# Optimization experiments

Hardware: AMD Instinct MI355X
Metric: run time of the kernel (lower is better)

The kernel has to match this reference:

```python
import jax, jax.numpy as jnp
import numpy as np

H = 8  # num_heads
NEG = -1000000.0

def _ln(x, g, b):
    m = jnp.mean(x, axis=-1, keepdims=True)
    v = jnp.var(x, axis=-1, keepdims=True)
    return (x - m) / jnp.sqrt(v + 1e-5) * g + b


def setup_inputs() -> dict:
    key = jax.random.key(0)
    ks = jax.random.split(key, 24)
    B, T, D = 8, 1024, 1024
    Lt, Nt, K, Rt, E = 768, 77, 2, 512, 2048
    s = 0.02
    r = lambda i, shape: s * jax.random.normal(ks[i], shape, jnp.float32)
    return {
        "x": jax.random.normal(ks[0], (B, T, D), jnp.float32),
        "xf": jax.random.normal(ks[1], (B, Nt, Lt), jnp.float32),
        "emb": jax.random.normal(ks[2], (B, E), jnp.float32),
        "src_mask": jnp.ones((B, T, 1), jnp.float32),
        "cond_type": jax.random.randint(ks[3], (B, 1, 1), 0, 100),
        "re_motion": jax.random.normal(ks[4], (B, K, Rt, D), jnp.float32),
        "re_text": jax.random.normal(ks[5], (B, K, 1, D), jnp.float32),
        "re_mask": jnp.ones((B, K, Rt), jnp.float32),
        "ln_g": jnp.ones((D,)), "ln_b": jnp.zeros((D,)),
        "tln_g": jnp.ones((Lt,)), "tln_b": jnp.zeros((Lt,)),
        "rn1_g": jnp.ones((2 * D,)), "rn1_b": jnp.zeros((2 * D,)),
        "rn2_g": jnp.ones((D,)), "rn2_b": jnp.zeros((D,)),
        "Wq": r(6, (D, D)), "bq": jnp.zeros((D,)),
        "Wkt": r(7, (Lt, D)), "bkt": jnp.zeros((D,)),
        "Wvt": r(8, (Lt, D)), "bvt": jnp.zeros((D,)),
        "Wkm": r(9, (D, D)), "bkm": jnp.zeros((D,)),
        "Wvm": r(10, (D, D)), "bvm": jnp.zeros((D,)),
        "Wkr": r(11, (2 * D, D)), "bkr": jnp.zeros((D,)),
        "Wvr": r(12, (D, D)), "bvr": jnp.zeros((D,)),  # zero-init in original; random here for nontrivial math
        "We": r(13, (E, 2 * D)), "be": jnp.zeros((2 * D,)),
        "sln_g": jnp.ones((D,)), "sln_b": jnp.zeros((D,)),
        "Wo": r(14, (D, D)), "bo": jnp.zeros((D,)),  # zero-init in original
    }


def reference(x, xf, emb, src_mask, cond_type, re_motion, re_text, re_mask,
              ln_g, ln_b, tln_g, tln_b, rn1_g, rn1_b, rn2_g, rn2_b,
              Wq, bq, Wkt, bkt, Wvt, bvt, Wkm, bkm, Wvm, bvm,
              Wkr, bkr, Wvr, bvr, We, be, sln_g, sln_b, Wo, bo):
    B, T, D = x.shape
    K, Rt = re_motion.shape[1], re_motion.shape[2]

    norm_x = _ln(x, ln_g, ln_b)
    norm_xf = _ln(xf, tln_g, tln_b)
    query = norm_x @ Wq + bq  # (B,T,D)

    text_ct = (cond_type % 10 > 0).astype(x.dtype)   # (B,1,1)
    retr_ct = (cond_type // 10 > 0).astype(x.dtype)  # (B,1,1)
    re_mask_r = re_mask.reshape(B, -1, 1)            # (B,K*Rt,1)

    # retrieval key features: concat(motion, repeated text) along channels
    re_text_rep = jnp.broadcast_to(re_text, (B, K, Rt, D))
    re_feat_key = jnp.concatenate([re_motion, re_text_rep], axis=-1).reshape(B, -1, 2 * D)

    key_text = norm_xf @ Wkt + bkt + (1.0 - text_ct) * NEG
    key_retr = _ln(re_feat_key, rn1_g, rn1_b) @ Wkr + bkr \
        + (1.0 - retr_ct) * NEG + (1.0 - re_mask_r) * NEG
    key_motion = norm_x @ Wkm + bkm + (1.0 - src_mask) * NEG
    key = jnp.concatenate([key_text, key_retr, key_motion], axis=1)  # (B,N,D)
    N = key.shape[1]

    q = jax.nn.softmax(query.reshape(B, T, H, -1), axis=-1)  # softmax over head dim
    k = jax.nn.softmax(key.reshape(B, N, H, -1), axis=1)     # softmax over tokens

    value_text = (norm_xf @ Wvt + bvt) * text_ct
    value_retr = (_ln(re_motion.reshape(B, -1, D), rn2_g, rn2_b) @ Wvr + bvr) * retr_ct * re_mask_r
    value_motion = (norm_x @ Wvm + bvm) * src_mask
    v = jnp.concatenate([value_text, value_retr, value_motion], axis=1).reshape(B, N, H, -1)

    att = jnp.einsum('bnhd,bnhl->bhdl', k, v)          # (B,H,dh,dh)
    y = jnp.einsum('bthd,bhdl->bthl', q, att).reshape(B, T, D)

    # StylizationBlock: FiLM from time embedding, then zero-init out proj (eval: dropout = id)
    eo = jax.nn.silu(emb) @ We + be                    # (B,2D)
    scale, shift = jnp.split(eo[:, None, :], 2, axis=2)
    h = _ln(y, sln_g, sln_b) * (1.0 + scale) + shift
    h = jax.nn.silu(h) @ Wo + bo
    return x + h
```

## Files before the change

### kernel.cpp

```cpp
#include <hip/hip_runtime.h>
#include <hip/hip_bf16.h>
#include <math.h>

using bf16 = __hip_bfloat16;

typedef short s16x8 __attribute__((ext_vector_type(8)));
typedef short s16x4 __attribute__((ext_vector_type(4)));
typedef float f32x4 __attribute__((ext_vector_type(4)));

constexpr int Bc = 8, Tc = 1024, Dc = 1024, Hc = 8;
constexpr int NTc = 77, LTc = 768, KRc = 1024, Nc = 2125, Ec = 2048;
constexpr float NEGC = -1000000.0f;

constexpr int NP = 2128;
constexpr long SKT = (long)Dc * NP;

constexpr long F_STATS1 = 0;
constexpr long F_STATS2 = F_STATS1 + 16384;
constexpr long F_KEYADD = F_STATS2 + 16384;
constexpr long F_VALMUL = F_KEYADD + 17000;
constexpr long F_SILU   = F_VALMUL + 17000;
constexpr long F_EO     = F_SILU + 16384;
constexpr long F_ATT    = F_EO + 16384;
constexpr long F_END    = F_ATT + 1048576;
constexpr long KT_SZ   = (long)Bc * Dc * NP;
constexpr long B_NORMX = 0;
constexpr long B_Q     = B_NORMX + 8388608;
constexpr long B_KT    = B_Q + 8388608;
constexpr long B_VT    = B_KT + KT_SZ;
constexpr long B_NXF   = B_VT + KT_SZ;
constexpr long B_WQ    = B_NXF + 473088;
constexpr long B_WKM   = B_WQ + 1048576;
constexpr long B_WVM   = B_WKM + 1048576;
constexpr long B_WKT   = B_WVM + 1048576;
constexpr long B_WVT   = B_WKT + 786432;
constexpr long B_WKR   = B_WVT + 786432;
constexpr long B_WVR   = B_WKR + 2097152;
constexpr long B_WO    = B_WVR + 1048576;
constexpr long B_END   = B_WO + 1048576;
constexpr size_t WS_NEED = (size_t)F_END * 4 + (size_t)B_END * 2;

__device__ __forceinline__ float b2f(bf16 v) { return __bfloat162float(v); }
__device__ __forceinline__ bf16 f2b(float v) { return __float2bfloat16(v); }
__device__ __forceinline__ short f2s(float v) {
    bf16 h = __float2bfloat16(v);
    return *reinterpret_cast<short*>(&h);
}
__device__ __forceinline__ float us2f(unsigned short u) {
    bf16 h = *reinterpret_cast<bf16*>(&u);
    return __bfloat162float(h);
}
__device__ __forceinline__ void storef(float* p, float v) { *p = v; }
__device__ __forceinline__ void storef(bf16* p, float v) { *p = __float2bfloat16(v); }

typedef __attribute__((address_space(1))) const unsigned int gu32;
typedef __attribute__((address_space(3))) unsigned int lu32;
__device__ __forceinline__ void gl_lds16(const void* g, void* l) {
    __builtin_amdgcn_global_load_lds((gu32*)g, (lu32*)l, 16, 0, 0);
}

__device__ __forceinline__ float2 block_sum2(float s, float s2) {
    #pragma unroll
    for (int off = 32; off > 0; off >>= 1) {
        s  += __shfl_down(s, off, 64);
        s2 += __shfl_down(s2, off, 64);
    }
    __shared__ float sh[4], sh2[4];
    int w = threadIdx.x >> 6, lane = threadIdx.x & 63;
    if (lane == 0) { sh[w] = s; sh2[w] = s2; }
    __syncthreads();
    s = sh[0] + sh[1] + sh[2] + sh[3];
    s2 = sh2[0] + sh2[1] + sh2[2] + sh2[3];
    return make_float2(s, s2);
}

template <typename TO>
__global__ __launch_bounds__(256) void ln_rows(const float* __restrict__ in,
                                               const float* __restrict__ g,
                                               const float* __restrict__ b,
                                               TO* __restrict__ out, int C) {
    long row = blockIdx.x;
    const float* x = in + row * (long)C;
    TO* o = out + row * (long)C;
    float s = 0.f, s2 = 0.f;
    for (int c = threadIdx.x; c < C; c += 256) { float v = x[c]; s += v; s2 += v * v; }
    float2 r = block_sum2(s, s2);
    float mean = r.x / C;
    float var = r.y / C - mean * mean;
    float inv = rsqrtf(var + 1e-5f);
    for (int c = threadIdx.x; c < C; c += 256)
        storef(&o[c], (x[c] - mean) * inv * g[c] + b[c]);
}

__global__ __launch_bounds__(256) void ln_stats_both(const float* __restrict__ motion,
                                                     const float* __restrict__ text,
                                                     float* __restrict__ stats1,
                                                     float* __restrict__ stats2) {
    long row = blockIdx.x;
    const float* m = motion + row * 1024;
    const float* tx = text + (row >> 9) * 1024;
    float s = 0.f, s2 = 0.f;
    for (int c = threadIdx.x; c < 1024; c += 256) { float v = m[c]; s += v; s2 += v * v; }
    float2 rm = block_sum2(s, s2);
    __syncthreads();
    float st = 0.f, st2 = 0.f;
    for (int c = threadIdx.x; c < 1024; c += 256) { float v = tx[c]; st += v; st2 += v * v; }
    float2 rt = block_sum2(st, st2);
    if (threadIdx.x == 0) {
        float mean2 = rm.x / 1024.f;
        float var2 = rm.y / 1024.f - mean2 * mean2;
        stats2[2 * row] = mean2;
        stats2[2 * row + 1] = rsqrtf(var2 + 1e-5f);
        float mean1 = (rm.x + rt.x) / 2048.f;
        float var1 = (rm.y + rt.y) / 2048.f - mean1 * mean1;
        stats1[2 * row] = mean1;
        stats1[2 * row + 1] = rsqrtf(var1 + 1e-5f);
    }
}

__device__ __forceinline__ s16x4 pack4(float4 v, float mean, float rstd, float4 g, float4 b) {
    s16x4 o;
    o[0] = f2s((v.x - mean) * rstd * g.x + b.x);
    o[1] = f2s((v.y - mean) * rstd * g.y + b.y);
    o[2] = f2s((v.z - mean) * rstd * g.z + b.z);
    o[3] = f2s((v.w - mean) * rstd * g.w + b.w);
    return o;
}
__global__ __launch_bounds__(256) void materialize_ren(
    const float* __restrict__ motion, const float* __restrict__ text,
    const float* __restrict__ stats1, const float* __restrict__ stats2,
    const float* __restrict__ g1, const float* __restrict__ b1,
    const float* __restrict__ g2, const float* __restrict__ b2,
    bf16* __restrict__ ren1, bf16* __restrict__ ren2) {
    long row = blockIdx.x;
    int c = threadIdx.x * 4;
    const float* mrow = motion + row * 1024;
    const float* trow = text + (row >> 9) * 1024;
    float m1 = stats1[2 * row], r1 = stats1[2 * row + 1];
    float m2 = stats2[2 * row], r2 = stats2[2 * row + 1];
    float4 mv = *(const float4*)(mrow + c);
    float4 tv = *(const float4*)(trow + c);
    float4 g1m = *(const float4*)(g1 + c),        b1m = *(const float4*)(b1 + c);
    float4 g1t = *(const float4*)(g1 + 1024 + c), b1t = *(const float4*)(b1 + 1024 + c);
    float4 g2m = *(const float4*)(g2 + c),        b2m = *(const float4*)(b2 + c);
    *(s16x4*)((short*)ren1 + row * 2048 + c)        = pack4(mv, m1, r1, g1m, b1m);
    *(s16x4*)((short*)ren1 + row * 2048 + 1024 + c) = pack4(tv, m1, r1, g1t, b1t);
    *(s16x4*)((short*)ren2 + row * 1024 + c)        = pack4(mv, m2, r2, g2m, b2m);
}

__global__ __launch_bounds__(256) void prep_masks(const int* __restrict__ cond_type,
                                                  const float* __restrict__ src_mask,
                                                  const float* __restrict__ re_mask,
                                                  float* __restrict__ key_add,
                                                  float* __restrict__ val_mul) {
    int idx = blockIdx.x * 256 + threadIdx.x;
    if (idx >= Bc * Nc) return;
    int b = idx / Nc, n = idx % Nc;
    int ct = cond_type[b];
    float text_ct = ((ct % 10) > 0) ? 1.f : 0.f;
    float retr_ct = ((ct / 10) > 0) ? 1.f : 0.f;
    float add, mul;
    if (n < NTc) {
        add = (1.f - text_ct) * NEGC; mul = text_ct;
    } else if (n < NTc + KRc) {
        float rm = re_mask[b * KRc + (n - NTc)];
        add = (1.f - retr_ct) * NEGC + (1.f - rm) * NEGC;
        mul = retr_ct * rm;
    } else {
        float sm = src_mask[b * Tc + (n - NTc - KRc)];
        add = (1.f - sm) * NEGC; mul = sm;
    }
    key_add[idx] = add;
    val_mul[idx] = mul;
}

__global__ __launch_bounds__(256) void zero_tail(bf16* __restrict__ vT) {
    int row = blockIdx.x * 256 + threadIdx.x;
    if (row >= Bc * Dc) return;
    bf16* p = vT + (long)row * NP + Nc;
    p[0] = f2b(0.f); p[1] = f2b(0.f); p[2] = f2b(0.f);
}

__global__ __launch_bounds__(256) void transpose_all(
    const float* __restrict__ Wq,  const float* __restrict__ Wkt,
    const float* __restrict__ Wvt, const float* __restrict__ Wkm,
    const float* __restrict__ Wvm, const float* __restrict__ Wkr,
    const float* __restrict__ Wvr, const float* __restrict__ Wo,
    short* __restrict__ WtQ,  short* __restrict__ WtKT,
    short* __restrict__ WtVT, short* __restrict__ WtKM,
    short* __restrict__ WtVM, short* __restrict__ WtKR,
    short* __restrict__ WtVR, short* __restrict__ WtO) {
    __shared__ float t[32][33];
    int sy = blockIdx.y;
    const float* W; short* Wt; int K; int ky;
    if (sy < 32)       { W = Wq;  Wt = WtQ;  K = 1024; ky = sy; }
    else if (sy < 56)  { W = Wkt; Wt = WtKT; K = 768;  ky = sy - 32; }
    else if (sy < 80)  { W = Wvt; Wt = WtVT; K = 768;  ky = sy - 56; }
    else if (sy < 112) { W = Wkm; Wt = WtKM; K = 1024; ky = sy - 80; }
    else if (sy < 144) { W = Wvm; Wt = WtVM; K = 1024; ky = sy - 112; }
    else if (sy < 208) { W = Wkr; Wt = WtKR; K = 2048; ky = sy - 144; }
    else if (sy < 240) { W = Wvr; Wt = WtVR; K = 1024; ky = sy - 208; }
    else               { W = Wo;  Wt = WtO;  K = 1024; ky = sy - 240; }
    int n0 = blockIdx.x * 32, k0 = ky * 32;
    int tx = threadIdx.x & 31, ty = threadIdx.x >> 5;
    #pragma unroll
    for (int i = 0; i < 4; ++i)
        t[ty + i * 8][tx] = W[(long)(k0 + ty + i * 8) * 1024 + n0 + tx];
    __syncthreads();
    #pragma unroll
    for (int i = 0; i < 4; ++i)
        Wt[(long)(n0 + ty + i * 8) * K + k0 + tx] = f2s(t[tx][ty + i * 8]);
}

constexpr int LDK = 64;

__global__ __launch_bounds__(256) void gemm_mega(
    const short* __restrict__ norm_x, const short* __restrict__ ren1,
    const short* __restrict__ nxf,
    const short* __restrict__ WtQKVM, const short* __restrict__ WtKR,
    const short* __restrict__ WtTXT,
    const float* __restrict__ bq, const float* __restrict__ bkm,
    const float* __restrict__ bvm, const float* __restrict__ bkr,
    const float* __restrict__ bkt, const float* __restrict__ bvt,
    const float* __restrict__ key_add, const float* __restrict__ val_mul,
    bf16* __restrict__ q16, bf16* __restrict__ kT, bf16* __restrict__ vT) {
    int jid = blockIdx.x;
    int sect, tm, tn, K, M, lda, bb = 0;
    const short* A; const short* Bt;
    if (jid < 512) {
        sect = 0;
        int s = (jid & 7) * 64 + (jid >> 3);
        bb = s >> 6; int r = s & 63;
        tm = (r >> 3) * 128; tn = (r & 7) * 128;
        A = ren1 + (long)bb * KRc * 2048; lda = 2048; K = 2048; M = 1024;
        Bt = WtKR;
    } else if (jid < 2048) {
        sect = 1;
        int l = jid - 512;
        int s = (l & 7) * 192 + (l >> 3);
        tn = (s % 24) * 128; tm = (s / 24) * 128;
        A = norm_x; lda = 1024; K = 1024; M = 8192;
        Bt = WtQKVM;
    } else {
        sect = 2;
        int l = jid - 2048;
        bb = l >> 4; tn = (l & 15) * 128; tm = 0;
        A = nxf + (long)bb * NTc * LTc; lda = 768; K = 768; M = 77;
        Bt = WtTXT;
    }
    const int ldb = lda;
    const bool swap_ops = !(sect == 1 && tn < 1024);

    __shared__ __align__(16) short As[128 * LDK];
    __shared__ __align__(16) short Bs[128 * LDK];

    int tid = threadIdx.x;
    int lane = tid & 63, wid = tid >> 6;
    int wi = wid >> 1, wj = wid & 1;
    int l16 = lane & 15, quad = lane >> 4;

    f32x4 acc[4][4];
    #pragma unroll
    for (int i = 0; i < 4; ++i)
        #pragma unroll
        for (int j = 0; j < 4; ++j)
            acc[i][j] = (f32x4){0.f, 0.f, 0.f, 0.f};

    auto issue = [&](int k0) {
        #pragma unroll
        for (int p = 0; p < 4; ++p) {
            int e = p * 256 + tid;
            int row = e >> 3, c8 = e & 7;
            int gm = tm + row;
            if (gm >= M) gm = M - 1;
            gl_lds16(A + (long)gm * lda + k0 + c8 * 8, &As[row * LDK + c8 * 8]);
            gl_lds16(Bt + (long)(tn + row) * ldb + k0 + c8 * 8, &Bs[row * LDK + c8 * 8]);
        }
    };

    issue(0);
    int kt = 0;
    while (true) {
        __syncthreads();
        #pragma unroll
        for (int kk = 0; kk < 2; ++kk) {
            s16x8 af[4], bfr[4];
            #pragma unroll
            for (int i = 0; i < 4; ++i)
                af[i] = *(const s16x8*)&As[(wi * 64 + i * 16 + l16) * LDK + kk * 32 + quad * 8];
            #pragma unroll
            for (int j = 0; j < 4; ++j)
                bfr[j] = *(const s16x8*)&Bs[(wj * 64 + j * 16 + l16) * LDK + kk * 32 + quad * 8];
            if (swap_ops) {
                #pragma unroll
                for (int i = 0; i < 4; ++i)
                    #pragma unroll
                    for (int j = 0; j < 4; ++j)
                        acc[i][j] = __builtin_amdgcn_mfma_f32_16x16x32_bf16(bfr[j], af[i], acc[i][j], 0, 0, 0);
            } else {
                #pragma unroll
                for (int i = 0; i < 4; ++i)
                    #pragma unroll
                    for (int j = 0; j < 4; ++j)
                        acc[i][j] = __builtin_amdgcn_mfma_f32_16x16x32_bf16(af[i], bfr[j], acc[i][j], 0, 0, 0);
            }
        }
        int nxt = kt + 64;
        if (nxt >= K) break;
        __syncthreads();
        issue(nxt);
        kt = nxt;
    }

    if (sect == 1 && tn < 1024) {
        #pragma unroll
        for (int i = 0; i < 4; ++i) {
            #pragma unroll
            for (int r = 0; r < 4; ++r) {
                int gm = tm + wi * 64 + i * 16 + quad * 4 + r;
                #pragma unroll
                for (int j = 0; j < 4; ++j) {
                    int gn = tn + wj * 64 + j * 16 + l16;
                    q16[(long)gm * Dc + gn] = f2b(acc[i][j][r] + bq[gn]);
                }
            }
        }
    } else if (sect == 1) {
        int sec = tn >> 10, fn0 = tn & 1023;
        const float* bias = (sec == 1) ? bkm : bvm;
        bf16* C = (sec == 1) ? kT : vT;
        #pragma unroll
        for (int j = 0; j < 4; ++j) {
            #pragma unroll
            for (int r = 0; r < 4; ++r) {
                int feat = fn0 + wj * 64 + j * 16 + quad * 4 + r;
                float bf_ = bias[feat];
                #pragma unroll
                for (int i = 0; i < 4; ++i) {
                    int gm = tm + wi * 64 + i * 16 + l16;
                    int b = gm >> 10, tok = gm & 1023;
                    int mi = b * Nc + NTc + KRc + tok;
                    float v = acc[i][j][r] + bf_;
                    if (sec == 1) v += key_add[mi];
                    else          v *= val_mul[mi];
                    C[(long)b * SKT + (long)feat * NP + NTc + KRc + tok] = f2b(v);
                }
            }
        }
    } else if (sect == 0) {
        const float* rmask = key_add + bb * Nc + NTc;
        bf16* C = kT + (long)bb * SKT + NTc;
        #pragma unroll
        for (int j = 0; j < 4; ++j) {
            #pragma unroll
            for (int r = 0; r < 4; ++r) {
                int feat = tn + wj * 64 + j * 16 + quad * 4 + r;
                float bf_ = bkr[feat];
                #pragma unroll
                for (int i = 0; i < 4; ++i) {
                    int tok = tm + wi * 64 + i * 16 + l16;
                    C[(long)feat * NP + tok] = f2b(acc[i][j][r] + bf_ + rmask[tok]);
                }
            }
        }
    } else {
        int sec = tn >> 10, fn0 = tn & 1023;
        const float* bias = sec ? bvt : bkt;
        const float* rmask = (sec ? val_mul : key_add) + bb * Nc;
        bf16* C = (sec ? vT : kT) + (long)bb * SKT;
        #pragma unroll
        for (int j = 0; j < 4; ++j) {
            #pragma unroll
            for (int r = 0; r < 4; ++r) {
                int feat = fn0 + wj * 64 + j * 16 + quad * 4 + r;
                float bf_ = bias[feat];
                #pragma unroll
                for (int i = 0; i < 4; ++i) {
                    int tok = wi * 64 + i * 16 + l16;
                    if (tok >= NTc) continue;
                    float v = acc[i][j][r] + bf_;
                    if (sec) v *= rmask[tok];
                    else     v += rmask[tok];
                    C[(long)feat * NP + tok] = f2b(v);
                }
            }
        }
    }
}

__global__ __launch_bounds__(256) void gemm_vr(
    const short* __restrict__ ren2, const short* __restrict__ WtVR,
    const float* __restrict__ bvr, const float* __restrict__ val_mul,
    bf16* __restrict__ vT) {
    int s = (blockIdx.x & 7) * 64 + (blockIdx.x >> 3);
    int b = s >> 6; int r = s & 63;
    const int tm = (r >> 3) * 128;
    const int tn = (r & 7) * 128;
    const short* A = ren2 + (long)b * KRc * 1024;
    const float* rmask = val_mul + b * Nc + NTc;
    bf16* C = vT + (long)b * SKT + NTc;

    __shared__ __align__(16) short As[128 * LDK];
    __shared__ __align__(16) short Bs[128 * LDK];

    int tid = threadIdx.x;
    int lane = tid & 63, wid = tid >> 6;
    int wi = wid >> 1, wj = wid & 1;
    int l16 = lane & 15, quad = lane >> 4;

    f32x4 acc[4][4];
    #pragma unroll
    for (int i = 0; i < 4; ++i)
        #pragma unroll
        for (int j = 0; j < 4; ++j)
            acc[i][j] = (f32x4){0.f, 0.f, 0.f, 0.f};

    auto issue = [&](int k0) {
        #pragma unroll
        for (int p = 0; p < 4; ++p) {
            int e = p * 256 + tid;
            int row = e >> 3, c8 = e & 7;
            gl_lds16(A + (long)(tm + row) * 1024 + k0 + c8 * 8, &As[row * LDK + c8 * 8]);
            gl_lds16(WtVR + (long)(tn + row) * 1024 + k0 + c8 * 8, &Bs[row * LDK + c8 * 8]);
        }
    };

    issue(0);
    int kt = 0;
    while (true) {
        __syncthreads();
        #pragma unroll
        for (int kk = 0; kk < 2; ++kk) {
            s16x8 af[4], bfr[4];
            #pragma unroll
            for (int i = 0; i < 4; ++i)
                af[i] = *(const s16x8*)&As[(wi * 64 + i * 16 + l16) * LDK + kk * 32 + quad * 8];
            #pragma unroll
            for (int j = 0; j < 4; ++j)
                bfr[j] = *(const s16x8*)&Bs[(wj * 64 + j * 16 + l16) * LDK + kk * 32 + quad * 8];
            #pragma unroll
            for (int i = 0; i < 4; ++i)
                #pragma unroll
                for (int j = 0; j < 4; ++j)
                    acc[i][j] = __builtin_amdgcn_mfma_f32_16x16x32_bf16(bfr[j], af[i], acc[i][j], 0, 0, 0);
        }
        int nxt = kt + 64;
        if (nxt >= 1024) break;
        __syncthreads();
        issue(nxt);
        kt = nxt;
    }

    #pragma unroll
    for (int j = 0; j < 4; ++j) {
        #pragma unroll
        for (int r2 = 0; r2 < 4; ++r2) {
            int feat = tn + wj * 64 + j * 16 + quad * 4 + r2;
            float bf_ = bvr[feat];
            #pragma unroll
            for (int i = 0; i < 4; ++i) {
                int tok = tm + wi * 64 + i * 16 + l16;
                C[(long)feat * NP + tok] = f2b((acc[i][j][r2] + bf_) * rmask[tok]);
            }
        }
    }
}

template <typename TC>
__global__ __launch_bounds__(256) void gemm_bt(
    const short* __restrict__ A, int lda,
    const short* __restrict__ Bt, int ldb,
    const float* __restrict__ bias,
    const float* __restrict__ addC, int ldac,
    TC* __restrict__ C, int ldc, int K) {
    int nx = gridDim.x;
    int nwg = nx * gridDim.y;
    int lin = blockIdx.y * nx + blockIdx.x;
    int bx = blockIdx.x, by = blockIdx.y;
    if ((nwg & 7) == 0) {
        int chunk = nwg >> 3;
        int swz = (lin & 7) * chunk + (lin >> 3);
        bx = swz % nx; by = swz / nx;
    }
    const int tm = by * 128;
    const int tn = bx * 128;

    __shared__ __align__(16) short As[128 * LDK];
    __shared__ __align__(16) short Bs[128 * LDK];

    int tid = threadIdx.x;
    int lane = tid & 63, wid = tid >> 6;
    int wi = wid >> 1, wj = wid & 1;
    int l16 = lane & 15, quad = lane >> 4;

    f32x4 acc[4][4];
    #pragma unroll
    for (int i = 0; i < 4; ++i)
        #pragma unroll
        for (int j = 0; j < 4; ++j)
            acc[i][j] = (f32x4){0.f, 0.f, 0.f, 0.f};

    auto issue = [&](int k0) {
        #pragma unroll
        for (int p = 0; p < 4; ++p) {
            int e = p * 256 + tid;
            int row = e >> 3, c8 = e & 7;
            gl_lds16(A + (long)(tm + row) * lda + k0 + c8 * 8, &As[row * LDK + c8 * 8]);
            gl_lds16(Bt + (long)(tn + row) * ldb + k0 + c8 * 8, &Bs[row * LDK + c8 * 8]);
        }
    };

    issue(0);
    int kt = 0;
    while (true) {
        __syncthreads();
        #pragma unroll
        for (int kk = 0; kk < 2; ++kk) {
            s16x8 af[4], bfr[4];
            #pragma unroll
            for (int i = 0; i < 4; ++i)
                af[i] = *(const s16x8*)&As[(wi * 64 + i * 16 + l16) * LDK + kk * 32 + quad * 8];
            #pragma unroll
            for (int j = 0; j < 4; ++j)
                bfr[j] = *(const s16x8*)&Bs[(wj * 64 + j * 16 + l16) * LDK + kk * 32 + quad * 8];
            #pragma unroll
            for (int i = 0; i < 4; ++i)
                #pragma unroll
                for (int j = 0; j < 4; ++j)
                    acc[i][j] = __builtin_amdgcn_mfma_f32_16x16x32_bf16(af[i], bfr[j], acc[i][j], 0, 0, 0);
        }
        int nxt = kt + 64;
        if (nxt >= K) break;
        __syncthreads();
        issue(nxt);
        kt = nxt;
    }

    #pragma unroll
    for (int i = 0; i < 4; ++i) {
        #pragma unroll
        for (int r = 0; r < 4; ++r) {
            int gm = tm + wi * 64 + i * 16 + quad * 4 + r;
            #pragma unroll
            for (int j = 0; j < 4; ++j) {
                int gn = tn + wj * 64 + j * 16 + l16;
                float v = acc[i][j][r] + bias[gn];
                if (addC) v += addC[(long)gm * ldac + gn];
                storef(&C[(long)gm * ldc + gn], v);
            }
        }
    }
}

__global__ __launch_bounds__(256) void eo_partial(const float* __restrict__ emb,
                                                  const float* __restrict__ We,
                                                  float* __restrict__ part) {
    int nb = blockIdx.x;
    int ks = blockIdx.y;
    int n = nb * 256 + threadIdx.x;
    int k0 = ks * 64;
    __shared__ float a_s[8][64];
    for (int idx = threadIdx.x; idx < 512; idx += 256) {
        int b = idx >> 6, kk = idx & 63;
        float v = emb[b * 2048 + k0 + kk];
        a_s[b][kk] = v / (1.f + expf(-v));
    }
    __syncthreads();
    float acc[8] = {};
    for (int kk = 0; kk < 64; ++kk) {
        float w = We[(long)(k0 + kk) * 2048 + n];
        #pragma unroll
        for (int b = 0; b < 8; ++b) acc[b] = fmaf(a_s[b][kk], w, acc[b]);
    }
    #pragma unroll
    for (int b = 0; b < 8; ++b) part[((long)ks * 8 + b) * 2048 + n] = acc[b];
}

__global__ __launch_bounds__(256) void eo_reduce(const float* __restrict__ part,
                                                 const float* __restrict__ be,
                                                 float* __restrict__ eo) {
    int idx = blockIdx.x * 256 + threadIdx.x;
    int n = idx & 2047, b = idx >> 11;
    float s = be[n];
    #pragma unroll 8
    for (int ks = 0; ks < 32; ++ks) s += part[((long)ks * 8 + b) * 2048 + n];
    eo[idx] = s;
}

__global__ __launch_bounds__(256) void softmax_head(bf16* __restrict__ q) {
    long row = (long)blockIdx.x * 4 + (threadIdx.x >> 6);
    int lane = threadIdx.x & 63;
    bf16* p = q + row * 128 + lane * 2;
    float v0 = b2f(p[0]), v1 = b2f(p[1]);
    float mx = fmaxf(v0, v1);
    #pragma unroll
    for (int off = 32; off > 0; off >>= 1) mx = fmaxf(mx, __shfl_xor(mx, off, 64));
    float e0 = expf(v0 - mx), e1 = expf(v1 - mx);
    float s = e0 + e1;
    #pragma unroll
    for (int off = 32; off > 0; off >>= 1) s += __shfl_xor(s, off, 64);
    float inv = 1.f / s;
    p[0] = f2b(e0 * inv);
    p[1] = f2b(e1 * inv);
}

__global__ __launch_bounds__(256) void ksm_rows(const bf16* __restrict__ kT,
                                                float* __restrict__ cs_m,
                                                float* __restrict__ cs_inv) {
    int row = blockIdx.x * 4 + (threadIdx.x >> 6);
    int lane = threadIdx.x & 63;
    const s16x8* p8 = (const s16x8*)(kT + (long)row * NP);
    float m = -3.0e38f;
    for (int c = lane; c < NP / 8; c += 64) {
        s16x8 raw = p8[c];
        int n0 = c * 8;
        #pragma unroll
        for (int j = 0; j < 8; ++j)
            if (n0 + j < Nc) m = fmaxf(m, us2f((unsigned short)raw[j]));
    }
    #pragma unroll
    for (int off = 32; off > 0; off >>= 1) m = fmaxf(m, __shfl_xor(m, off, 64));
    float s = 0.f;
    for (int c = lane; c < NP / 8; c += 64) {
        s16x8 raw = p8[c];
        int n0 = c * 8;
        #pragma unroll
        for (int j = 0; j < 8; ++j)
            if (n0 + j < Nc) s += __expf(us2f((unsigned short)raw[j]) - m);
    }
    #pragma unroll
    for (int off = 32; off > 0; off >>= 1) s += __shfl_xor(s, off, 64);
    if (lane == 0) { cs_m[row] = m; cs_inv[row] = 1.f / s; }
}

constexpr int ATT_SPLIT = 4;
__global__ __launch_bounds__(256) void att_gemm(const bf16* __restrict__ kTb,
                                                const bf16* __restrict__ vTb,
                                                const float* __restrict__ cs_m,
                                                float* __restrict__ att_part) {
    int bh = blockIdx.x;
    int split = blockIdx.y;
    int b = bh >> 3, h = bh & 7;
    const short* A  = (const short*)kTb + ((long)b * 1024 + h * 128) * NP;
    const short* Bt = (const short*)vTb + ((long)b * 1024 + h * 128) * NP;
    float* ap = att_part + ((long)split * 64 + bh) * 16384;

    __shared__ __align__(16) short As[128 * LDK];
    __shared__ __align__(16) short Bs[128 * LDK];
    __shared__ float ms[128];

    int tid = threadIdx.x;
    if (tid < 128) ms[tid] = cs_m[(long)b * 1024 + h * 128 + tid];

    int lane = tid & 63, wid = tid >> 6;
    int wi = wid >> 1, wj = wid & 1;
    int l16 = lane & 15, quad = lane >> 4;

    f32x4 acc[4][4];
    #pragma unroll
    for (int i = 0; i < 4; ++i)
        #pragma unroll
        for (int j = 0; j < 4; ++j)
            acc[i][j] = (f32x4){0.f, 0.f, 0.f, 0.f};

    uint4 pa[4];
    auto computeA = [&](int k0) {
        #pragma unroll
        for (int p = 0; p < 4; ++p) {
            int e = p * 256 + tid;
            int row = e >> 3, c8 = e & 7;
            int n0 = k0 + c8 * 8;
            union { short s[8]; uint4 u; } pk;
            if (n0 >= Nc) {
                pk.u = (uint4){0u, 0u, 0u, 0u};
            } else {
                float m = ms[row];
                s16x8 raw = *(const s16x8*)(A + (long)row * NP + n0);
                #pragma unroll
                for (int j = 0; j < 8; ++j) {
                    float v = (n0 + j < Nc) ? __expf(us2f((unsigned short)raw[j]) - m) : 0.f;
                    pk.s[j] = f2s(v);
                }
            }
            pa[p] = pk.u;
        }
    };
    auto issueB = [&](int k0) {
        #pragma unroll
        for (int p = 0; p < 4; ++p) {
            int e = p * 256 + tid;
            int row = e >> 3, c8 = e & 7;
            int n0 = k0 + c8 * 8;
            if (n0 > NP - 8) n0 = NP - 8;
            gl_lds16(Bt + (long)row * NP + n0, &Bs[row * LDK + c8 * 8]);
        }
    };
    auto storeA = [&]() {
        #pragma unroll
        for (int p = 0; p < 4; ++p) {
            int e = p * 256 + tid;
            int row = e >> 3, c8 = e & 7;
            *(uint4*)&As[row * LDK + c8 * 8] = pa[p];
        }
    };

    int st = (split < 2) ? split * 9 : 18 + (split - 2) * 8;
    int cnt = (split < 2) ? 9 : 8;
    int kt = st * 64;
    int kend = kt + cnt * 64;

    __syncthreads();
    issueB(kt);
    computeA(kt);
    storeA();
    while (true) {
        __syncthreads();
        #pragma unroll
        for (int kk = 0; kk < 2; ++kk) {
            s16x8 af[4], bfr[4];
            #pragma unroll
            for (int i = 0; i < 4; ++i)
                af[i] = *(const s16x8*)&As[(wi * 64 + i * 16 + l16) * LDK + kk * 32 + quad * 8];
            #pragma unroll
            for (int j = 0; j < 4; ++j)
                bfr[j] = *(const s16x8*)&Bs[(wj * 64 + j * 16 + l16) * LDK + kk * 32 + quad * 8];
            #pragma unroll
            for (int i = 0; i < 4; ++i)
                #pragma unroll
                for (int j = 0; j < 4; ++j)
                    acc[i][j] = __builtin_amdgcn_mfma_f32_16x16x32_bf16(bfr[j], af[i], acc[i][j], 0, 0, 0);
        }
        int nxt = kt + 64;
        if (nxt >= kend) break;
        computeA(nxt);
        __syncthreads();
        issueB(nxt);
        storeA();
        kt = nxt;
    }

    #pragma unroll
    for (int j = 0; j < 4; ++j) {
        #pragma unroll
        for (int r = 0; r < 4; ++r) {
            int l = wj * 64 + j * 16 + quad * 4 + r;
            #pragma unroll
            for (int i = 0; i < 4; ++i) {
                int d = wi * 64 + i * 16 + l16;
                ap[l * 128 + d] = acc[i][j][r];
            }
        }
    }
}

__global__ __launch_bounds__(256) void reduce_att_t(const float* __restrict__ att_part,
                                                    const float* __restrict__ cs_inv,
                                                    bf16* __restrict__ attT) {
    long idx = (long)blockIdx.x * 256 + threadIdx.x;
    if (idx >= (long)64 * 16384) return;
    float s = 0.f;
    #pragma unroll
    for (int sp = 0; sp < ATT_SPLIT; ++sp) s += att_part[(long)sp * 64 * 16384 + idx];
    int bh = (int)(idx >> 14);
    int d = (int)(idx & 127);
    int b = bh >> 3, h = bh & 7;
    attT[idx] = f2b(s * cs_inv[b * Dc + h * 128 + d]);
}

__global__ __launch_bounds__(256) void y_gemm(const bf16* __restrict__ q,
                                              const bf16* __restrict__ attT,
                                              bf16* __restrict__ y) {
    int bh = blockIdx.y;
    int b = bh >> 3, h = bh & 7;
    const short* A  = (const short*)q + (long)b * Tc * Dc + h * 128;
    const short* Bt = (const short*)attT + (long)bh * 16384;
    bf16* yb = y + (long)b * Tc * Dc + h * 128;
    int tm = blockIdx.x * 128;

    __shared__ __align__(16) short As[128 * 128];
    __shared__ __align__(16) short Bs[128 * 128];
    int tid = threadIdx.x;
    #pragma unroll
    for (int p = 0; p < 8; ++p) {
        int e = p * 256 + tid;
        int row = e >> 4, c8 = e & 15;
        gl_lds16(A + (long)(tm + row) * Dc + c8 * 8, &As[row * 128 + c8 * 8]);
        gl_lds16(Bt + row * 128 + c8 * 8, &Bs[row * 128 + c8 * 8]);
    }
    int lane = tid & 63, wid = tid >> 6;
    int wi = wid >> 1, wj = wid & 1;
    int l16 = lane & 15, quad = lane >> 4;
    f32x4 acc[4][4];
    #pragma unroll
    for (int i = 0; i < 4; ++i)
        #pragma unroll
        for (int j = 0; j < 4; ++j)
            acc[i][j] = (f32x4){0.f, 0.f, 0.f, 0.f};
    __syncthreads();
    #pragma unroll
    for (int kk = 0; kk < 4; ++kk) {
        s16x8 af[4], bfr[4];
        #pragma unroll
        for (int i = 0; i < 4; ++i)
            af[i] = *(const s16x8*)&As[(wi * 64 + i * 16 + l16) * 128 + kk * 32 + quad * 8];
        #pragma unroll
        for (int j = 0; j < 4; ++j)
            bfr[j] = *(const s16x8*)&Bs[(wj * 64 + j * 16 + l16) * 128 + kk * 32 + quad * 8];
        #pragma unroll
        for (int i = 0; i < 4; ++i)
            #pragma unroll
            for (int j = 0; j < 4; ++j)
                acc[i][j] = __builtin_amdgcn_mfma_f32_16x16x32_bf16(af[i], bfr[j], acc[i][j], 0, 0, 0);
    }
    #pragma unroll
    for (int i = 0; i < 4; ++i) {
        #pragma unroll
        for (int r = 0; r < 4; ++r) {
            int gm = tm + wi * 64 + i * 16 + quad * 4 + r;
            #pragma unroll
            for (int j = 0; j < 4; ++j) {
                int gn = wj * 64 + j * 16 + l16;
                yb[(long)gm * Dc + gn] = f2b(acc[i][j][r]);
            }
        }
    }
}

__global__ __launch_bounds__(256) void film_kernel(const bf16* __restrict__ y,
                                                   const float* __restrict__ eo,
                                                   const float* __restrict__ g,
                                                   const float* __restrict__ bta,
                                                   bf16* __restrict__ s) {
    long row = blockIdx.x;
    int b = (int)(row >> 10);
    const bf16* yr = y + row * Dc;
    float sum = 0.f, sum2 = 0.f;
    for (int c = threadIdx.x; c < Dc; c += 256) { float v = b2f(yr[c]); sum += v; sum2 += v * v; }
    float2 r = block_sum2(sum, sum2);
    float mean = r.x / Dc;
    float var = r.y / Dc - mean * mean;
    float inv = rsqrtf(var + 1e-5f);
    const float* sc = eo + (long)b * 2048;
    const float* sf = sc + 1024;
    bf16* so = s + row * Dc;
    for (int c = threadIdx.x; c < Dc; c += 256) {
        float v = (b2f(yr[c]) - mean) * inv * g[c] + bta[c];
        v = v * (1.f + sc[c]) + sf[c];
        so[c] = f2b(v / (1.f + expf(-v)));
    }
}

extern "C" void kernel_launch(void* const* d_in, const int* in_sizes, int n_in,
                              void* d_out, int out_size, void* d_ws, size_t ws_size,
                              hipStream_t stream) {
    if (ws_size < WS_NEED) return;

    const float* x         = (const float*)d_in[0];
    const float* xf        = (const float*)d_in[1];
    const float* emb       = (const float*)d_in[2];
    const float* src_mask  = (const float*)d_in[3];
    const int*   cond_type = (const int*)d_in[4];
    const float* re_motion = (const float*)d_in[5];
    const float* re_text   = (const float*)d_in[6];
    const float* re_mask   = (const float*)d_in[7];
    const float* ln_g  = (const float*)d_in[8];
    const float* ln_b  = (const float*)d_in[9];
    const float* tln_g = (const float*)d_in[10];
    const float* tln_b = (const float*)d_in[11];
    const float* rn1_g = (const float*)d_in[12];
    const float* rn1_b = (const float*)d_in[13];
    const float* rn2_g = (const float*)d_in[14];
    const float* rn2_b = (const float*)d_in[15];
    const float* Wq  = (const float*)d_in[16];
    const float* bq  = (const float*)d_in[17];
    const float* Wkt = (const float*)d_in[18];
    const float* bkt = (const float*)d_in[19];
    const float* Wvt = (const float*)d_in[20];
    const float* bvt = (const float*)d_in[21];
    const float* Wkm = (const float*)d_in[22];
    const float* bkm = (const float*)d_in[23];
    const float* Wvm = (const float*)d_in[24];
    const float* bvm = (const float*)d_in[25];
    const float* Wkr = (const float*)d_in[26];
    const float* bkr = (const float*)d_in[27];
    const float* Wvr = (const float*)d_in[28];
    const float* bvr = (const float*)d_in[29];
    const float* We  = (const float*)d_in[30];
    const float* be  = (const float*)d_in[31];
    const float* sln_g = (const float*)d_in[32];
    const float* sln_b = (const float*)d_in[33];
    const float* Wo  = (const float*)d_in[34];
    const float* bo  = (const float*)d_in[35];

    float* ws = (float*)d_ws;
    float* stats1   = ws + F_STATS1;
    float* stats2   = ws + F_STATS2;
    float* key_add  = ws + F_KEYADD;
    float* val_mul  = ws + F_VALMUL;
    float* cs_m     = ws + F_SILU;
    float* cs_inv   = cs_m + Bc * Dc;
    float* eo       = ws + F_EO;
    bf16*  attT     = (bf16*)(ws + F_ATT);
    bf16* wb = (bf16*)(ws + F_END);
    bf16* norm_x16 = wb + B_NORMX;
    bf16* q16      = wb + B_Q;
    bf16* kT16     = wb + B_KT;
    bf16* vT16     = wb + B_VT;
    bf16* nxf16    = wb + B_NXF;
    short* WtQ  = (short*)(wb + B_WQ);
    short* WtKM = (short*)(wb + B_WKM);
    short* WtVM = (short*)(wb + B_WVM);
    short* WtKT = (short*)(wb + B_WKT);
    short* WtVT = (short*)(wb + B_WVT);
    short* WtKR = (short*)(wb + B_WKR);
    short* WtVR = (short*)(wb + B_WVR);
    short* WtO  = (short*)(wb + B_WO);
    float* att_part = (float*)(wb + B_NORMX);
    bf16* y16 = wb + B_NORMX;
    bf16* s16 = q16;
    float* eo_part = (float*)(wb + B_VT);
    bf16* ren1 = (bf16*)d_out;
    bf16* ren2 = q16;

    float* out = (float*)d_out;

    ln_rows<bf16><<<dim3(Bc * Tc), dim3(256), 0, stream>>>(x, ln_g, ln_b, norm_x16, Dc);
    ln_rows<bf16><<<dim3(Bc * NTc), dim3(256), 0, stream>>>(xf, tln_g, tln_b, nxf16, LTc);
    ln_stats_both<<<dim3(Bc * KRc), dim3(256), 0, stream>>>(re_motion, re_text, stats1, stats2);

    prep_masks<<<dim3((Bc * Nc + 255) / 256), dim3(256), 0, stream>>>(
        cond_type, src_mask, re_mask, key_add, val_mul);
    zero_tail<<<dim3((Bc * Dc + 255) / 256), dim3(256), 0, stream>>>(vT16);

    transpose_all<<<dim3(32, 272), dim3(256), 0, stream>>>(
        Wq, Wkt, Wvt, Wkm, Wvm, Wkr, Wvr, Wo,
        WtQ, WtKT, WtVT, WtKM, WtVM, WtKR, WtVR, WtO);

    materialize_ren<<<dim3(Bc * KRc), dim3(256), 0, stream>>>(
        re_motion, re_text, stats1, stats2, rn1_g, rn1_b, rn2_g, rn2_b, ren1, ren2);

    gemm_vr<<<dim3(512), dim3(256), 0, stream>>>(
        (const short*)ren2, WtVR, bvr, val_mul, vT16);

    gemm_mega<<<dim3(2176), dim3(256), 0, stream>>>(
        (const short*)norm_x16, (const short*)ren1, (const short*)nxf16,
        WtQ, WtKR, WtKT,
        bq, bkm, bvm, bkr, bkt, bvt,
        key_add, val_mul, q16, kT16, vT16);

    softmax_head<<<dim3(Bc * Tc * Hc / 4), dim3(256), 0, stream>>>(q16);
    ksm_rows<<<dim3(Bc * Dc / 4), dim3(256), 0, stream>>>(kT16, cs_m, cs_inv);

    att_gemm<<<dim3(Bc * Hc, ATT_SPLIT), dim3(256), 0, stream>>>(kT16, vT16, cs_m, att_part);
    reduce_att_t<<<dim3((64 * 16384 + 255) / 256), dim3(256), 0, stream>>>(att_part, cs_inv, attT);

    y_gemm<<<dim3(Tc / 128, Bc * Hc), dim3(256), 0, stream>>>(q16, attT, y16);

    eo_partial<<<dim3(8, 32), dim3(256), 0, stream>>>(emb, We, eo_part);
    eo_reduce<<<dim3(64), dim3(256), 0, stream>>>(eo_part, be, eo);

    film_kernel<<<dim3(Bc * Tc), dim3(256), 0, stream>>>(y16, eo, sln_g, sln_b, s16);

    gemm_bt<float><<<dim3(8, 64), dim3(256), 0, stream>>>(
        (const short*)s16, 1024, WtO, 1024, bo, x, 1024, out, 1024, 1024);
}
```

Measured before the change: 636.8 us.

## Fuse LN stats with materialization, merge small kernels, fold Vr GEMM into mega

Several unrelated changes land together. Retrieval LayerNorm statistics are now computed inside the materialize kernel, and the mask prep and tail-zero kernels are merged into one launch. When the workspace is large enough, the value-retrieval GEMM becomes a fourth section of the mega GEMM, writing ren2 to a separate buffer. The output GEMM is specialized to 128x64 tiles for more blocks, and the attention split goes from 4 to 8 with partials stored in the output buffer. The goal is fewer launches and better occupancy, at the cost of more partial-reduction traffic and a larger workspace.

```diff
diff --git a/kernel.cpp b/kernel.cpp
--- a/kernel.cpp
+++ b/kernel.cpp
@@ -38,7 +38,10 @@
 constexpr long B_WVR   = B_WKR + 2097152;
 constexpr long B_WO    = B_WVR + 1048576;
 constexpr long B_END   = B_WO + 1048576;
+constexpr long B_REN2  = B_END;
+constexpr long REN2_SZ = 8388608;
 constexpr size_t WS_NEED = (size_t)F_END * 4 + (size_t)B_END * 2;
+constexpr size_t WS_BIG  = (size_t)F_END * 4 + (size_t)(B_END + REN2_SZ) * 2;
 
 __device__ __forceinline__ float b2f(bf16 v) { return __bfloat162float(v); }
 __device__ __forceinline__ bf16 f2b(float v) { return __float2bfloat16(v); }
@@ -92,32 +95,6 @@
         storef(&o[c], (x[c] - mean) * inv * g[c] + b[c]);
 }
 
-__global__ __launch_bounds__(256) void ln_stats_both(const float* __restrict__ motion,
-                                                     const float* __restrict__ text,
-                                                     float* __restrict__ stats1,
-                                                     float* __restrict__ stats2) {
-    long row = blockIdx.x;
-    const float* m = motion + row * 1024;
-    const float* tx = text + (row >> 9) * 1024;
-    float s = 0.f, s2 = 0.f;
-    for (int c = threadIdx.x; c < 1024; c += 256) { float v = m[c]; s += v; s2 += v * v; }
-    float2 rm = block_sum2(s, s2);
-    __syncthreads();
-    float st = 0.f, st2 = 0.f;
-    for (int c = threadIdx.x; c < 1024; c += 256) { float v = tx[c]; st += v; st2 += v * v; }
-    float2 rt = block_sum2(st, st2);
-    if (threadIdx.x == 0) {
-        float mean2 = rm.x / 1024.f;
-        float var2 = rm.y / 1024.f - mean2 * mean2;
-        stats2[2 * row] = mean2;
-        stats2[2 * row + 1] = rsqrtf(var2 + 1e-5f);
-        float mean1 = (rm.x + rt.x) / 2048.f;
-        float var1 = (rm.y + rt.y) / 2048.f - mean1 * mean1;
-        stats1[2 * row] = mean1;
-        stats1[2 * row + 1] = rsqrtf(var1 + 1e-5f);
-    }
-}
-
 __device__ __forceinline__ s16x4 pack4(float4 v, float mean, float rstd, float4 g, float4 b) {
     s16x4 o;
     o[0] = f2s((v.x - mean) * rstd * g.x + b.x);
@@ -126,9 +103,9 @@
     o[3] = f2s((v.w - mean) * rstd * g.w + b.w);
     return o;
 }
-__global__ __launch_bounds__(256) void materialize_ren(
+
+__global__ __launch_bounds__(256) void ln_mat(
     const float* __restrict__ motion, const float* __restrict__ text,
-    const float* __restrict__ stats1, const float* __restrict__ stats2,
     const float* __restrict__ g1, const float* __restrict__ b1,
     const float* __restrict__ g2, const float* __restrict__ b2,
     bf16* __restrict__ ren1, bf16* __restrict__ ren2) {
@@ -136,49 +113,62 @@
     int c = threadIdx.x * 4;
     const float* mrow = motion + row * 1024;
     const float* trow = text + (row >> 9) * 1024;
-    float m1 = stats1[2 * row], r1 = stats1[2 * row + 1];
-    float m2 = stats2[2 * row], r2 = stats2[2 * row + 1];
     float4 mv = *(const float4*)(mrow + c);
     float4 tv = *(const float4*)(trow + c);
+    float sm = mv.x + mv.y + mv.z + mv.w;
+    float sm2 = mv.x * mv.x + mv.y * mv.y + mv.z * mv.z + mv.w * mv.w;
+    float2 rm = block_sum2(sm, sm2);
+    __syncthreads();
+    float st = tv.x + tv.y + tv.z + tv.w;
+    float st2 = tv.x * tv.x + tv.y * tv.y + tv.z * tv.z + tv.w * tv.w;
+    float2 rt = block_sum2(st, st2);
+    float mean2 = rm.x / 1024.f;
+    float var2 = rm.y / 1024.f - mean2 * mean2;
+    float r2 = rsqrtf(var2 + 1e-5f);
+    float mean1 = (rm.x + rt.x) / 2048.f;
+    float var1 = (rm.y + rt.y) / 2048.f - mean1 * mean1;
+    float r1 = rsqrtf(var1 + 1e-5f);
     float4 g1m = *(const float4*)(g1 + c),        b1m = *(const float4*)(b1 + c);
     float4 g1t = *(const float4*)(g1 + 1024 + c), b1t = *(const float4*)(b1 + 1024 + c);
     float4 g2m = *(const float4*)(g2 + c),        b2m = *(const float4*)(b2 + c);
-    *(s16x4*)((short*)ren1 + row * 2048 + c)        = pack4(mv, m1, r1, g1m, b1m);
-    *(s16x4*)((short*)ren1 + row * 2048 + 1024 + c) = pack4(tv, m1, r1, g1t, b1t);
-    *(s16x4*)((short*)ren2 + row * 1024 + c)        = pack4(mv, m2, r2, g2m, b2m);
-}
-
-__global__ __launch_bounds__(256) void prep_masks(const int* __restrict__ cond_type,
-                                                  const float* __restrict__ src_mask,
-                                                  const float* __restrict__ re_mask,
-                                                  float* __restrict__ key_add,
-                                                  float* __restrict__ val_mul) {
-    int idx = blockIdx.x * 256 + threadIdx.x;
-    if (idx >= Bc * Nc) return;
-    int b = idx / Nc, n = idx % Nc;
-    int ct = cond_type[b];
-    float text_ct = ((ct % 10) > 0) ? 1.f : 0.f;
-    float retr_ct = ((ct / 10) > 0) ? 1.f : 0.f;
-    float add, mul;
-    if (n < NTc) {
-        add = (1.f - text_ct) * NEGC; mul = text_ct;
-    } else if (n < NTc + KRc) {
-        float rm = re_mask[b * KRc + (n - NTc)];
-        add = (1.f - retr_ct) * NEGC + (1.f - rm) * NEGC;
-        mul = retr_ct * rm;
+    *(s16x4*)((short*)ren1 + row * 2048 + c)        = pack4(mv, mean1, r1, g1m, b1m);
+    *(s16x4*)((short*)ren1 + row * 2048 + 1024 + c) = pack4(tv, mean1, r1, g1t, b1t);
+    *(s16x4*)((short*)ren2 + row * 1024 + c)        = pack4(mv, mean2, r2, g2m, b2m);
+}
+
+__global__ __launch_bounds__(256) void prep_zero(const int* __restrict__ cond_type,
+                                                 const float* __restrict__ src_mask,
+                                                 const float* __restrict__ re_mask,
+                                                 float* __restrict__ key_add,
+                                                 float* __restrict__ val_mul,
+                                                 bf16* __restrict__ vT) {
+    int bid = blockIdx.x;
+    if (bid < 67) {
+        int idx = bid * 256 + threadIdx.x;
+        if (idx >= Bc * Nc) return;
+        int b = idx / Nc, n = idx % Nc;
+        int ct = cond_type[b];
+        float text_ct = ((ct % 10) > 0) ? 1.f : 0.f;
+        float retr_ct = ((ct / 10) > 0) ? 1.f : 0.f;
+        float add, mul;
+        if (n < NTc) {
+            add = (1.f - text_ct) * NEGC; mul = text_ct;
+        } else if (n < NTc + KRc) {
+            float rm = re_mask[b * KRc + (n - NTc)];
+            add = (1.f - retr_ct) * NEGC + (1.f - rm) * NEGC;
+            mul = retr_ct * rm;
+        } else {
+            float sm = src_mask[b * Tc + (n - NTc - KRc)];
+            add = (1.f - sm) * NEGC; mul = sm;
+        }
+        key_add[idx] = add;
+        val_mul[idx] = mul;
     } else {
-        float sm = src_mask[b * Tc + (n - NTc - KRc)];
-        add = (1.f - sm) * NEGC; mul = sm;
-    }
-    key_add[idx] = add;
-    val_mul[idx] = mul;
-}
-
-__global__ __launch_bounds__(256) void zero_tail(bf16* __restrict__ vT) {
-    int row = blockIdx.x * 256 + threadIdx.x;
-    if (row >= Bc * Dc) return;
-    bf16* p = vT + (long)row * NP + Nc;
-    p[0] = f2b(0.f); p[1] = f2b(0.f); p[2] = f2b(0.f);
+        int row = (bid - 67) * 256 + threadIdx.x;
+        if (row >= Bc * Dc) return;
+        bf16* p = vT + (long)row * NP + Nc;
+        p[0] = f2b(0.f); p[1] = f2b(0.f); p[2] = f2b(0.f);
+    }
 }
 
 __global__ __launch_bounds__(256) void transpose_all(
@@ -216,11 +206,12 @@
 
 __global__ __launch_bounds__(256) void gemm_mega(
     const short* __restrict__ norm_x, const short* __restrict__ ren1,
-    const short* __restrict__ nxf,
+    const short* __restrict__ ren2, const short* __restrict__ nxf,
     const short* __restrict__ WtQKVM, const short* __restrict__ WtKR,
-    const short* __restrict__ WtTXT,
+    const short* __restrict__ WtVR, const short* __restrict__ WtTXT,
     const float* __restrict__ bq, const float* __restrict__ bkm,
     const float* __restrict__ bvm, const float* __restrict__ bkr,
+    const float* __restrict__ bvr,
     const float* __restrict__ bkt, const float* __restrict__ bvt,
     const float* __restrict__ key_add, const float* __restrict__ val_mul,
     bf16* __restrict__ q16, bf16* __restrict__ kT, bf16* __restrict__ vT) {
@@ -241,12 +232,20 @@
         tn = (s % 24) * 128; tm = (s / 24) * 128;
         A = norm_x; lda = 1024; K = 1024; M = 8192;
         Bt = WtQKVM;
-    } else {
+    } else if (jid < 2176) {
         sect = 2;
         int l = jid - 2048;
         bb = l >> 4; tn = (l & 15) * 128; tm = 0;
         A = nxf + (long)bb * NTc * LTc; lda = 768; K = 768; M = 77;
         Bt = WtTXT;
+    } else {
+        sect = 3;
+        int l = jid - 2176;
+        int s = (l & 7) * 64 + (l >> 3);
+        bb = s >> 6; int r = s & 63;
+        tm = (r >> 3) * 128; tn = (r & 7) * 128;
+        A = ren2 + (long)bb * KRc * 1024; lda = 1024; K = 1024; M = 1024;
+        Bt = WtVR;
     }
     const int ldb = lda;
     const bool swap_ops = !(sect == 1 && tn < 1024);
@@ -360,6 +359,22 @@
                 for (int i = 0; i < 4; ++i) {
                     int tok = tm + wi * 64 + i * 16 + l16;
                     C[(long)feat * NP + tok] = f2b(acc[i][j][r] + bf_ + rmask[tok]);
+                }
+            }
+        }
+    } else if (sect == 3) {
+        const float* rmask = val_mul + bb * Nc + NTc;
+        bf16* C = vT + (long)bb * SKT + NTc;
+        #pragma unroll
+        for (int j = 0; j < 4; ++j) {
+            #pragma unroll
+            for (int r = 0; r < 4; ++r) {
+                int feat = tn + wj * 64 + j * 16 + quad * 4 + r;
+                float bf_ = bvr[feat];
+                #pragma unroll
+                for (int i = 0; i < 4; ++i) {
+                    int tok = tm + wi * 64 + i * 16 + l16;
+                    C[(long)feat * NP + tok] = f2b((acc[i][j][r] + bf_) * rmask[tok]);
                 }
             }
         }
@@ -466,38 +481,27 @@
     }
 }
 
-template <typename TC>
-__global__ __launch_bounds__(256) void gemm_bt(
-    const short* __restrict__ A, int lda,
-    const short* __restrict__ Bt, int ldb,
-    const float* __restrict__ bias,
-    const float* __restrict__ addC, int ldac,
-    TC* __restrict__ C, int ldc, int K) {
-    int nx = gridDim.x;
-    int nwg = nx * gridDim.y;
-    int lin = blockIdx.y * nx + blockIdx.x;
-    int bx = blockIdx.x, by = blockIdx.y;
-    if ((nwg & 7) == 0) {
-        int chunk = nwg >> 3;
-        int swz = (lin & 7) * chunk + (lin >> 3);
-        bx = swz % nx; by = swz / nx;
-    }
-    const int tm = by * 128;
-    const int tn = bx * 128;
+__global__ __launch_bounds__(256) void gemm_out(
+    const short* __restrict__ A, const short* __restrict__ Bt,
+    const float* __restrict__ bias, const float* __restrict__ addC,
+    float* __restrict__ C) {
+    int s = (blockIdx.x & 7) * 128 + (blockIdx.x >> 3);
+    const int tm = (s >> 4) * 128;
+    const int tn = (s & 15) * 64;
 
     __shared__ __align__(16) short As[128 * LDK];
-    __shared__ __align__(16) short Bs[128 * LDK];
+    __shared__ __align__(16) short Bs[64 * LDK];
 
     int tid = threadIdx.x;
     int lane = tid & 63, wid = tid >> 6;
     int wi = wid >> 1, wj = wid & 1;
     int l16 = lane & 15, quad = lane >> 4;
 
-    f32x4 acc[4][4];
+    f32x4 acc[4][2];
     #pragma unroll
     for (int i = 0; i < 4; ++i)
         #pragma unroll
-        for (int j = 0; j < 4; ++j)
+        for (int j = 0; j < 2; ++j)
             acc[i][j] = (f32x4){0.f, 0.f, 0.f, 0.f};
 
     auto issue = [&](int k0) {
@@ -505,8 +509,13 @@
         for (int p = 0; p < 4; ++p) {
             int e = p * 256 + tid;
             int row = e >> 3, c8 = e & 7;
-            gl_lds16(A + (long)(tm + row) * lda + k0 + c8 * 8, &As[row * LDK + c8 * 8]);
-            gl_lds16(Bt + (long)(tn + row) * ldb + k0 + c8 * 8, &Bs[row * LDK + c8 * 8]);
+            gl_lds16(A + (long)(tm + row) * 1024 + k0 + c8 * 8, &As[row * LDK + c8 * 8]);
+        }
+        #pragma unroll
+        for (int p = 0; p < 2; ++p) {
+            int e = p * 256 + tid;
+            int row = e >> 3, c8 = e & 7;
+            gl_lds16(Bt + (long)(tn + row) * 1024 + k0 + c8 * 8, &Bs[row * LDK + c8 * 8]);
         }
     };
 
@@ -516,21 +525,21 @@
         __syncthreads();
         #pragma unroll
         for (int kk = 0; kk < 2; ++kk) {
-            s16x8 af[4], bfr[4];
+            s16x8 af[4], bfr[2];
             #pragma unroll
             for (int i = 0; i < 4; ++i)
                 af[i] = *(const s16x8*)&As[(wi * 64 + i * 16 + l16) * LDK + kk * 32 + quad * 8];
             #pragma unroll
-            for (int j = 0; j < 4; ++j)
-                bfr[j] = *(const s16x8*)&Bs[(wj * 64 + j * 16 + l16) * LDK + kk * 32 + quad * 8];
+            for (int j = 0; j < 2; ++j)
+                bfr[j] = *(const s16x8*)&Bs[(wj * 32 + j * 16 + l16) * LDK + kk * 32 + quad * 8];
             #pragma unroll
             for (int i = 0; i < 4; ++i)
                 #pragma unroll
-                for (int j = 0; j < 4; ++j)
+                for (int j = 0; j < 2; ++j)
                     acc[i][j] = __builtin_amdgcn_mfma_f32_16x16x32_bf16(af[i], bfr[j], acc[i][j], 0, 0, 0);
         }
         int nxt = kt + 64;
-        if (nxt >= K) break;
+        if (nxt >= 1024) break;
         __syncthreads();
         issue(nxt);
         kt = nxt;
@@ -542,11 +551,9 @@
         for (int r = 0; r < 4; ++r) {
             int gm = tm + wi * 64 + i * 16 + quad * 4 + r;
             #pragma unroll
-            for (int j = 0; j < 4; ++j) {
-                int gn = tn + wj * 64 + j * 16 + l16;
-                float v = acc[i][j][r] + bias[gn];
-                if (addC) v += addC[(long)gm * ldac + gn];
-                storef(&C[(long)gm * ldc + gn], v);
+            for (int j = 0; j < 2; ++j) {
+                int gn = tn + wj * 32 + j * 16 + l16;
+                C[(long)gm * 1024 + gn] = acc[i][j][r] + bias[gn] + addC[(long)gm * 1024 + gn];
             }
         }
     }
@@ -633,7 +640,7 @@
     if (lane == 0) { cs_m[row] = m; cs_inv[row] = 1.f / s; }
 }
 
-constexpr int ATT_SPLIT = 4;
+constexpr int ATT_SPLIT = 8;
 __global__ __launch_bounds__(256) void att_gemm(const bf16* __restrict__ kTb,
                                                 const bf16* __restrict__ vTb,
                                                 const float* __restrict__ cs_m,
@@ -704,8 +711,8 @@
         }
     };
 
-    int st = (split < 2) ? split * 9 : 18 + (split - 2) * 8;
-    int cnt = (split < 2) ? 9 : 8;
+    int st = (split < 2) ? split * 5 : 10 + (split - 2) * 4;
+    int cnt = (split < 2) ? 5 : 4;
     int kt = st * 64;
     int kend = kt + cnt * 64;
 
@@ -854,6 +861,7 @@
                               void* d_out, int out_size, void* d_ws, size_t ws_size,
                               hipStream_t stream) {
     if (ws_size < WS_NEED) return;
+    const bool big = ws_size >= WS_BIG;
 
     const float* x         = (const float*)d_in[0];
     const float* xf        = (const float*)d_in[1];
@@ -893,8 +901,6 @@
     const float* bo  = (const float*)d_in[35];
 
     float* ws = (float*)d_ws;
-    float* stats1   = ws + F_STATS1;
-    float* stats2   = ws + F_STATS2;
     float* key_add  = ws + F_KEYADD;
     float* val_mul  = ws + F_VALMUL;
     float* cs_m     = ws + F_SILU;
@@ -915,37 +921,35 @@
     short* WtKR = (short*)(wb + B_WKR);
     short* WtVR = (short*)(wb + B_WVR);
     short* WtO  = (short*)(wb + B_WO);
-    float* att_part = (float*)(wb + B_NORMX);
     bf16* y16 = wb + B_NORMX;
     bf16* s16 = q16;
     float* eo_part = (float*)(wb + B_VT);
     bf16* ren1 = (bf16*)d_out;
-    bf16* ren2 = q16;
+    float* att_part = (float*)d_out;
+    bf16* ren2 = big ? (wb + B_REN2) : q16;
 
     float* out = (float*)d_out;
 
     ln_rows<bf16><<<dim3(Bc * Tc), dim3(256), 0, stream>>>(x, ln_g, ln_b, norm_x16, Dc);
     ln_rows<bf16><<<dim3(Bc * NTc), dim3(256), 0, stream>>>(xf, tln_g, tln_b, nxf16, LTc);
-    ln_stats_both<<<dim3(Bc * KRc), dim3(256), 0, stream>>>(re_motion, re_text, stats1, stats2);
-
-    prep_masks<<<dim3((Bc * Nc + 255) / 256), dim3(256), 0, stream>>>(
-        cond_type, src_mask, re_mask, key_add, val_mul);
-    zero_tail<<<dim3((Bc * Dc + 255) / 256), dim3(256), 0, stream>>>(vT16);
+    ln_mat<<<dim3(Bc * KRc), dim3(256), 0, stream>>>(
+        re_motion, re_text, rn1_g, rn1_b, rn2_g, rn2_b, ren1, ren2);
+
+    prep_zero<<<dim3(99), dim3(256), 0, stream>>>(
+        cond_type, src_mask, re_mask, key_add, val_mul, vT16);
 
     transpose_all<<<dim3(32, 272), dim3(256), 0, stream>>>(
         Wq, Wkt, Wvt, Wkm, Wvm, Wkr, Wvr, Wo,
         WtQ, WtKT, WtVT, WtKM, WtVM, WtKR, WtVR, WtO);
 
-    materialize_ren<<<dim3(Bc * KRc), dim3(256), 0, stream>>>(
-        re_motion, re_text, stats1, stats2, rn1_g, rn1_b, rn2_g, rn2_b, ren1, ren2);
-
-    gemm_vr<<<dim3(512), dim3(256), 0, stream>>>(
-        (const short*)ren2, WtVR, bvr, val_mul, vT16);
-
-    gemm_mega<<<dim3(2176), dim3(256), 0, stream>>>(
-        (const short*)norm_x16, (const short*)ren1, (const short*)nxf16,
-        WtQ, WtKR, WtKT,
-        bq, bkm, bvm, bkr, bkt, bvt,
+    if (!big)
+        gemm_vr<<<dim3(512), dim3(256), 0, stream>>>(
+            (const short*)ren2, WtVR, bvr, val_mul, vT16);
+
+    gemm_mega<<<dim3(big ? 2688 : 2176), dim3(256), 0, stream>>>(
+        (const short*)norm_x16, (const short*)ren1, (const short*)ren2,
+        (const short*)nxf16, WtQ, WtKR, WtVR, WtKT,
+        bq, bkm, bvm, bkr, bvr, bkt, bvt,
         key_add, val_mul, q16, kT16, vT16);
 
     softmax_head<<<dim3(Bc * Tc * Hc / 4), dim3(256), 0, stream>>>(q16);
@@ -961,6 +965,6 @@
 
     film_kernel<<<dim3(Bc * Tc), dim3(256), 0, stream>>>(y16, eo, sln_g, sln_b, s16);
 
-    gemm_bt<float><<<dim3(8, 64), dim3(256), 0, stream>>>(
-        (const short*)s16, 1024, WtO, 1024, bo, x, 1024, out, 1024, 1024);
-}
+    gemm_out<<<dim3(1024), dim3(256), 0, stream>>>(
+        (const short*)s16, WtO, bo, x, out);
+}
```

Measured after the change: 583.2 us. -8.4%, faster.
